# Performance work log

Measured on AMD Instinct MI355X. Metric: run time of the kernel, lower is better.

Reference implementation:

```python
import jax, jax.numpy as jnp
import numpy as np
from jax import lax

D = 512      # inter_dim
E = 768      # expand_dim
S = 256      # squeeze_dim
BUCKET = 64
N_BLOCK = 6

def layernorm(x, g, b, eps):
    m = jnp.mean(x, axis=-1, keepdims=True)
    v = jnp.mean(jnp.square(x - m), axis=-1, keepdims=True)
    return (x - m) / jnp.sqrt(v + eps) * g + b

def setup_inputs():
    key = jax.random.key(0)
    ks = jax.random.split(key, 12)
    B, N, IN = 4, 4096, 768
    def rn(k, shape, scale):
        return jax.random.normal(k, shape, dtype=jnp.float32) * scale
    return {
        "xs": jax.random.normal(ks[0], (B, N, IN), dtype=jnp.float32),
        # in1: Linear(IN, D) + LayerNorm(eps=1e-8) + LeakyReLU(0.1)
        "W_in": rn(ks[1], (IN, D), IN ** -0.5), "b_in": jnp.zeros(D),
        "ln_in_g": jnp.ones(D), "ln_in_b": jnp.zeros(D),
        # 6 GAU (FlashQuadAttention) blocks, params stacked on leading axis
        "blk_ln_g": jnp.ones((N_BLOCK, D)), "blk_ln_b": jnp.zeros((N_BLOCK, D)),
        "blk_Wuv": rn(ks[2], (N_BLOCK, D, 2 * E + S), D ** -0.5),
        "blk_buv": jnp.zeros((N_BLOCK, 2 * E + S)),
        "blk_gamma": jnp.ones((N_BLOCK, 2, S)) + rn(ks[3], (N_BLOCK, 2, S), 0.02),
        "blk_beta": rn(ks[4], (N_BLOCK, 2, S), 0.02),
        "blk_Wo": rn(ks[5], (N_BLOCK, E, D), E ** -0.5),
        "blk_bo": jnp.zeros((N_BLOCK, D)),
        # tr_layer (applied inside tree loop)
        "tr_W": rn(ks[6], (D, D), D ** -0.5), "tr_b": jnp.zeros(D),
        "tr_a": jnp.full((), 1e-6, dtype=jnp.float32),
        # out1 = TransLayer + Linear(D, out_dim)
        "tr2_W": rn(ks[7], (D, D), D ** -0.5), "tr2_b": jnp.zeros(D),
        "tr2_a": jnp.full((), 1e-6, dtype=jnp.float32),
        "out_W": rn(ks[8], (D, 2), D ** -0.5), "out_b": jnp.zeros(2),
    }

def reference(xs, W_in, b_in, ln_in_g, ln_in_b,
              blk_ln_g, blk_ln_b, blk_Wuv, blk_buv, blk_gamma, blk_beta,
              blk_Wo, blk_bo, tr_W, tr_b, tr_a, tr2_W, tr2_b, tr2_a,
              out_W, out_b):
    def subnet(h):  # h: [n_buckets, BUCKET, D]
        def step(h, p):
            lg, lb, Wuv, buv, gam, bet, Wo, bo = p
            n = layernorm(h, lg, lb, 1e-5)
            uvb = jax.nn.silu(n @ Wuv + buv)
            u, v, base = uvb[..., :E], uvb[..., E:2 * E], uvb[..., 2 * E:]
            q = base * gam[0] + bet[0]
            k = base * gam[1] + bet[1]
            Lq = h.shape[1]
            a = jnp.square(jax.nn.relu(jnp.einsum('gls,gms->glm', q, k) / Lq))
            o = jnp.einsum('glm,gme->gle', a, v) * u
            return h + o @ Wo + bo, None
        h, _ = lax.scan(step, h, (blk_ln_g, blk_ln_b, blk_Wuv, blk_buv,
                                  blk_gamma, blk_beta, blk_Wo, blk_bo))
        return h

    def tr_layer(x, W, b, a):
        return x + jax.nn.gelu(x @ W + b, approximate=False) * a

    def run_sample(x):  # x: [N, in_dim]
        h = layernorm(x @ W_in + b_in, ln_in_g, ln_in_b, 1e-8)
        h = jnp.where(h > 0, h, 0.1 * h)  # LeakyReLU(0.1)
        seq = h
        ys = []
        while seq.shape[0] > 1:  # static shapes -> unrolled tree levels
            ids = jnp.argsort(jnp.linalg.norm(seq, axis=-1))  # sort by L2 norm
            buckets = seq[ids].reshape(-1, BUCKET, D)
            gy = subnet(buckets).mean(axis=1)           # [n_buckets, D]
            ys.append(tr_layer(gy, tr_W, tr_b, tr_a).mean(axis=0))
            seq = gy
        return jnp.stack(ys, 0).mean(0)  # [D]

    y = jax.vmap(run_sample)(xs)          # [B, D]
    y = tr_layer(y, tr2_W, tr2_b, tr2_a)  # out1 TransLayer
    return y @ out_W + out_b              # [B, out_dim]
```

## Files before the change

kernel.cpp:

```cpp
#include <hip/hip_runtime.h>
#include <math.h>

#define R1C 16384

enum { OP_STORE = 0, OP_SILU = 1, OP_RESID = 2, OP_TR = 3 };

typedef _Float16 f16x8 __attribute__((ext_vector_type(8)));
typedef float f32x4 __attribute__((ext_vector_type(4)));

__device__ __forceinline__ float silu_f(float x) { return x / (1.0f + __expf(-x)); }
__device__ __forceinline__ float gelu_f(float x) {
  return 0.5f * x * (1.0f + erff(x * 0.70710678118654752f));
}

__device__ __forceinline__ void gll16(const void* g, const void* l) {
  __builtin_amdgcn_global_load_lds(
      (const __attribute__((address_space(1))) unsigned int*)g,
      (__attribute__((address_space(3))) unsigned int*)l, 16, 0, 0);
}


__global__ __launch_bounds__(512) void gemm_f16(
    const _Float16* __restrict__ A, int lda,
    const _Float16* __restrict__ Bt, int ldb,
    float* __restrict__ C, int ldc, int K,
    const float* __restrict__ bias, int mode,
    const int* __restrict__ ids)
{
  const int BUF = 128 * 32;
  __shared__ _Float16 As[2 * BUF];
  __shared__ _Float16 Bs[2 * BUF];
  int tid = threadIdx.x;
  int lane = tid & 63, w = tid >> 6;
  int wm = w >> 1, wn = w & 1;
  int row0 = blockIdx.y * 128, col0 = blockIdx.x * 128;

  int m0 = tid >> 2;
  int k0e = (((tid & 3) - (m0 >> 1)) & 3) * 8;
  const _Float16* gA0 = A + (size_t)(row0 + m0) * lda + k0e;
  const _Float16* gB0 = Bt + (size_t)(col0 + m0) * ldb + k0e;
  const _Float16* lA0 = As + (size_t)(w * 64) * 8;
  const _Float16* lB0 = Bs + (size_t)(w * 64) * 8;

  int mrow = lane & 15, quad = lane >> 4;
  const f16x8* aptr[2];
  const f16x8* bptr[4];
#pragma unroll
  for (int t = 0; t < 2; ++t) {
    int ml = wm * 32 + t * 16 + mrow;
    aptr[t] = (const f16x8*)(As + (size_t)(ml * 4 + ((quad + (ml >> 1)) & 3)) * 8);
  }
#pragma unroll
  for (int nt = 0; nt < 4; ++nt) {
    int nl = wn * 64 + nt * 16 + mrow;
    bptr[nt] = (const f16x8*)(Bs + (size_t)(nl * 4 + ((quad + (nl >> 1)) & 3)) * 8);
  }

  f32x4 acc[2][4] = {};

  gll16(gA0, lA0); gll16(gB0, lB0);
  gA0 += 32; gB0 += 32;

  for (int kt = 0; kt < K; kt += 32) {
    int cur = (kt >> 5) & 1;
    __syncthreads();
    if (kt + 32 < K) {
      int nx = cur ^ 1;
      gll16(gA0, lA0 + nx * BUF); gll16(gB0, lB0 + nx * BUF);
      gA0 += 32; gB0 += 32;
    }
    int fo = cur * (BUF / 8);
    f16x8 af[2], bfr[4];
#pragma unroll
    for (int t = 0; t < 2; ++t) af[t] = *(aptr[t] + fo);
#pragma unroll
    for (int nt = 0; nt < 4; ++nt) bfr[nt] = *(bptr[nt] + fo);
#pragma unroll
    for (int mt = 0; mt < 2; ++mt)
#pragma unroll
      for (int nt = 0; nt < 4; ++nt)
        acc[mt][nt] = __builtin_amdgcn_mfma_f32_16x16x32_f16(
            af[mt], bfr[nt], acc[mt][nt], 0, 0, 0);
  }

#pragma unroll
  for (int mt = 0; mt < 2; ++mt) {
#pragma unroll
    for (int nt = 0; nt < 4; ++nt) {
      int c = col0 + wn * 64 + nt * 16 + mrow;
      float bv = bias ? bias[c] : 0.0f;
#pragma unroll
      for (int reg = 0; reg < 4; ++reg) {
        int r = row0 + wm * 32 + mt * 16 + quad * 4 + reg;
        float val = acc[mt][nt][reg] + bv;
        if (mode == OP_STORE) {
          C[(size_t)r * ldc + c] = val;
        } else if (mode == OP_SILU) {
          C[(size_t)r * ldc + c] = silu_f(val);
        } else {
          int hr = ids ? ids[r] : r;
          C[(size_t)hr * ldc + c] += val;
        }
      }
    }
  }
}

__global__ __launch_bounds__(512) void gemm_f16_split(
    const _Float16* __restrict__ Ah, const _Float16* __restrict__ Al, int lda,
    const _Float16* __restrict__ Bh, const _Float16* __restrict__ Bl, int ldb,
    float* __restrict__ C, int ldc, int K, const float* __restrict__ bias)
{
  const int BUF = 128 * 32;
  __shared__ _Float16 AsH[2 * BUF], AsL[2 * BUF];
  __shared__ _Float16 BsH[2 * BUF], BsL[2 * BUF];
  int tid = threadIdx.x;
  int lane = tid & 63, w = tid >> 6;
  int wm = w >> 1, wn = w & 1;
  int row0 = blockIdx.y * 128, col0 = blockIdx.x * 128;

  int m0 = tid >> 2;
  int k0e = (((tid & 3) - (m0 >> 1)) & 3) * 8;
  size_t a0 = (size_t)(row0 + m0) * lda + k0e;
  size_t b0 = (size_t)(col0 + m0) * ldb + k0e;
  size_t l0 = (size_t)(w * 64) * 8;

  int mrow = lane & 15, quad = lane >> 4;
  size_t aoff[2], boff[4];
#pragma unroll
  for (int t = 0; t < 2; ++t) {
    int ml = wm * 32 + t * 16 + mrow;
    aoff[t] = (size_t)(ml * 4 + ((quad + (ml >> 1)) & 3)) * 8;
  }
#pragma unroll
  for (int nt = 0; nt < 4; ++nt) {
    int nl = wn * 64 + nt * 16 + mrow;
    boff[nt] = (size_t)(nl * 4 + ((quad + (nl >> 1)) & 3)) * 8;
  }

  f32x4 acc[2][4] = {};

  gll16(Ah + a0, AsH + l0); gll16(Al + a0, AsL + l0);
  gll16(Bh + b0, BsH + l0); gll16(Bl + b0, BsL + l0);
  a0 += 32; b0 += 32;

  for (int kt = 0; kt < K; kt += 32) {
    int cur = (kt >> 5) & 1;
    __syncthreads();
    if (kt + 32 < K) {
      size_t o = (size_t)(cur ^ 1) * BUF;
      gll16(Ah + a0, AsH + l0 + o); gll16(Al + a0, AsL + l0 + o);
      gll16(Bh + b0, BsH + l0 + o); gll16(Bl + b0, BsL + l0 + o);
      a0 += 32; b0 += 32;
    }
    size_t o = (size_t)cur * BUF;
    f16x8 ah[2], al_[2], bh[4], bl[4];
#pragma unroll
    for (int t = 0; t < 2; ++t) {
      ah[t]  = *(const f16x8*)(AsH + aoff[t] + o);
      al_[t] = *(const f16x8*)(AsL + aoff[t] + o);
    }
#pragma unroll
    for (int nt = 0; nt < 4; ++nt) {
      bh[nt] = *(const f16x8*)(BsH + boff[nt] + o);
      bl[nt] = *(const f16x8*)(BsL + boff[nt] + o);
    }
#pragma unroll
    for (int mt = 0; mt < 2; ++mt)
#pragma unroll
      for (int nt = 0; nt < 4; ++nt) {
        acc[mt][nt] = __builtin_amdgcn_mfma_f32_16x16x32_f16(
            ah[mt], bh[nt], acc[mt][nt], 0, 0, 0);
        acc[mt][nt] = __builtin_amdgcn_mfma_f32_16x16x32_f16(
            ah[mt], bl[nt], acc[mt][nt], 0, 0, 0);
        acc[mt][nt] = __builtin_amdgcn_mfma_f32_16x16x32_f16(
            al_[mt], bh[nt], acc[mt][nt], 0, 0, 0);
      }
  }

#pragma unroll
  for (int mt = 0; mt < 2; ++mt)
#pragma unroll
    for (int nt = 0; nt < 4; ++nt) {
      int c = col0 + wn * 64 + nt * 16 + mrow;
      float bv = bias ? bias[c] : 0.0f;
#pragma unroll
      for (int reg = 0; reg < 4; ++reg) {
        int r = row0 + wm * 32 + mt * 16 + quad * 4 + reg;
        C[(size_t)r * ldc + c] = acc[mt][nt][reg] + bv;
      }
    }
}

__global__ __launch_bounds__(512) void gemm_f16_uvb(
    const _Float16* __restrict__ A, int lda,
    const _Float16* __restrict__ Bt,
    int c0, int nu,
    _Float16* __restrict__ ub, _Float16* __restrict__ vb, float* __restrict__ baseb,
    int CH, int K, const float* __restrict__ buv)
{
  const int BUF = 128 * 32;
  __shared__ _Float16 As[2 * BUF];
  __shared__ _Float16 Bs[2 * BUF];
  int tid = threadIdx.x;
  int lane = tid & 63, w = tid >> 6;
  int wm = w >> 1, wn = w & 1;
  int row0 = blockIdx.y * 128;

  int x = blockIdx.x;
  int xl, regbase, ldc_, is_base = 0;
  _Float16* dst16 = nullptr;
  if (x < nu)            { xl = x;          regbase = c0;        dst16 = ub; ldc_ = CH; }
  else if (x < 2 * nu)   { xl = x - nu;     regbase = 768 + c0;  dst16 = vb; ldc_ = CH; }
  else                   { xl = x - 2 * nu; regbase = 1536;      is_base = 1; ldc_ = 256; }
  int brow0 = regbase + xl * 128;
  int dcol0 = xl * 128;

  int m0 = tid >> 2;
  int k0e = (((tid & 3) - (m0 >> 1)) & 3) * 8;
  const _Float16* gA0 = A + (size_t)(row0 + m0) * lda + k0e;
  const _Float16* gB0 = Bt + (size_t)(brow0 + m0) * 512 + k0e;
  const _Float16* lA0 = As + (size_t)(w * 64) * 8;
  const _Float16* lB0 = Bs + (size_t)(w * 64) * 8;

  int mrow = lane & 15, quad = lane >> 4;
  const f16x8* aptr[2];
  const f16x8* bptr[4];
#pragma unroll
  for (int t = 0; t < 2; ++t) {
    int ml = wm * 32 + t * 16 + mrow;
    aptr[t] = (const f16x8*)(As + (size_t)(ml * 4 + ((quad + (ml >> 1)) & 3)) * 8);
  }
#pragma unroll
  for (int nt = 0; nt < 4; ++nt) {
    int nl = wn * 64 + nt * 16 + mrow;
    bptr[nt] = (const f16x8*)(Bs + (size_t)(nl * 4 + ((quad + (nl >> 1)) & 3)) * 8);
  }

  f32x4 acc[2][4] = {};

  gll16(gA0, lA0); gll16(gB0, lB0);
  gA0 += 32; gB0 += 32;

  for (int kt = 0; kt < K; kt += 32) {
    int cur = (kt >> 5) & 1;
    __syncthreads();
    if (kt + 32 < K) {
      int nx = cur ^ 1;
      gll16(gA0, lA0 + nx * BUF); gll16(gB0, lB0 + nx * BUF);
      gA0 += 32; gB0 += 32;
    }
    int fo = cur * (BUF / 8);
    f16x8 af[2], bfr[4];
#pragma unroll
    for (int t = 0; t < 2; ++t) af[t] = *(aptr[t] + fo);
#pragma unroll
    for (int nt = 0; nt < 4; ++nt) bfr[nt] = *(bptr[nt] + fo);
#pragma unroll
    for (int mt = 0; mt < 2; ++mt)
#pragma unroll
      for (int nt = 0; nt < 4; ++nt)
        acc[mt][nt] = __builtin_amdgcn_mfma_f32_16x16x32_f16(
            af[mt], bfr[nt], acc[mt][nt], 0, 0, 0);
  }

#pragma unroll
  for (int mt = 0; mt < 2; ++mt) {
#pragma unroll
    for (int nt = 0; nt < 4; ++nt) {
      int lc = wn * 64 + nt * 16 + mrow;
      float bv = buv[brow0 + lc];
#pragma unroll
      for (int reg = 0; reg < 4; ++reg) {
        int r = row0 + wm * 32 + mt * 16 + quad * 4 + reg;
        float val = silu_f(acc[mt][nt][reg] + bv);
        if (is_base) baseb[(size_t)r * 256 + dcol0 + lc] = val;
        else         dst16[(size_t)r * ldc_ + dcol0 + lc] = (_Float16)val;
      }
    }
  }
}

__global__ __launch_bounds__(256) void attnapply_fused(
    const float* __restrict__ base, const float* __restrict__ gb,
    const float* __restrict__ bb, const _Float16* __restrict__ v,
    const _Float16* __restrict__ u, _Float16* __restrict__ t, int CH, int ech)
{
  __shared__ _Float16 smem[3 * 64 * 72];
  _Float16* qs = smem;
  _Float16* ks = smem + 64 * 72;
  _Float16* al = smem + 2 * 64 * 72;
  _Float16* vT = smem;

  int g = blockIdx.y, tid = threadIdx.x;
  int e_lo = blockIdx.x * ech, e_hi = e_lo + ech;
  int lane = tid & 63, w = tid >> 6;
  int mrow = lane & 15, quad = lane >> 4;
  int srow = tid >> 2, scol = (tid & 3) * 16;

  f32x4 acc[4] = {};
  for (int s0 = 0; s0 < 256; s0 += 64) {
    const float* bp = base + ((size_t)g * 64 + srow) * 256 + s0 + scol;
#pragma unroll
    for (int j4 = 0; j4 < 4; ++j4) {
      float4 xv = *(const float4*)(bp + j4 * 4);
      float xx[4] = {xv.x, xv.y, xv.z, xv.w};
#pragma unroll
      for (int j = 0; j < 4; ++j) {
        int s = s0 + scol + j4 * 4 + j;
        qs[srow * 72 + scol + j4 * 4 + j] = (_Float16)(xx[j] * gb[s] + bb[s]);
        ks[srow * 72 + scol + j4 * 4 + j] = (_Float16)(xx[j] * gb[256 + s] + bb[256 + s]);
      }
    }
    __syncthreads();
#pragma unroll
    for (int ks2 = 0; ks2 < 2; ++ks2) {
      f16x8 aq = *(const f16x8*)(qs + (w * 16 + mrow) * 72 + ks2 * 32 + quad * 8);
#pragma unroll
      for (int nt = 0; nt < 4; ++nt) {
        f16x8 bk = *(const f16x8*)(ks + (nt * 16 + mrow) * 72 + ks2 * 32 + quad * 8);
        acc[nt] = __builtin_amdgcn_mfma_f32_16x16x32_f16(aq, bk, acc[nt], 0, 0, 0);
      }
    }
    __syncthreads();
  }
#pragma unroll
  for (int nt = 0; nt < 4; ++nt)
#pragma unroll
    for (int reg = 0; reg < 4; ++reg) {
      float val = acc[nt][reg] * (1.0f / 64.0f);
      val = val > 0.0f ? val : 0.0f;
      val = val * val;
      al[(w * 16 + quad * 4 + reg) * 72 + nt * 16 + mrow] = (_Float16)val;
    }
  __syncthreads();

  for (int e0 = e_lo; e0 < e_hi; e0 += 64) {
    const _Float16* vp = v + ((size_t)g * 64 + srow) * CH + e0 + scol;
    f16x8 x0 = *(const f16x8*)vp;
    f16x8 x1 = *(const f16x8*)(vp + 8);
#pragma unroll
    for (int j = 0; j < 8; ++j) {
      vT[(scol + j) * 72 + srow] = x0[j];
      vT[(scol + 8 + j) * 72 + srow] = x1[j];
    }
    __syncthreads();
    f32x4 acc2[4] = {};
#pragma unroll
    for (int ks2 = 0; ks2 < 2; ++ks2) {
      f16x8 af = *(const f16x8*)(al + (w * 16 + mrow) * 72 + ks2 * 32 + quad * 8);
#pragma unroll
      for (int nt = 0; nt < 4; ++nt) {
        f16x8 bf = *(const f16x8*)(vT + (nt * 16 + mrow) * 72 + ks2 * 32 + quad * 8);
        acc2[nt] = __builtin_amdgcn_mfma_f32_16x16x32_f16(af, bf, acc2[nt], 0, 0, 0);
      }
    }
#pragma unroll
    for (int nt = 0; nt < 4; ++nt)
#pragma unroll
      for (int reg = 0; reg < 4; ++reg) {
        int row = w * 16 + quad * 4 + reg;
        int col = e0 + nt * 16 + mrow;
        size_t idx = ((size_t)g * 64 + row) * CH + col;
        t[idx] = (_Float16)(acc2[nt][reg] * (float)u[idx]);
      }
    __syncthreads();
  }
}

__global__ __launch_bounds__(256) void gemm_f32(
    const float* __restrict__ A, int lda,
    const float* __restrict__ B, int ldb,
    float* __restrict__ C, int ldc,
    int M, int N, int K,
    const float* __restrict__ bias, int mode,
    const int* __restrict__ ids,
    const float* __restrict__ X,
    const float* __restrict__ alpha)
{
  __shared__ float As[16][68];
  __shared__ float Bs[16][68];
  int tid = threadIdx.x;
  int tx = tid & 15, ty = tid >> 4;
  int col0 = blockIdx.x * 64, row0 = blockIdx.y * 64;
  float acc[4][4] = {};
  int arow = tid >> 2;
  int ak   = (tid & 3) * 4;
  int bk   = tid >> 4;
  int bn   = (tid & 15) * 4;

  for (int kt = 0; kt < K; kt += 16) {
    float4 av = make_float4(0.f, 0.f, 0.f, 0.f);
    if (row0 + arow < M)
      av = *(const float4*)&A[(size_t)(row0 + arow) * lda + kt + ak];
    As[ak + 0][arow] = av.x; As[ak + 1][arow] = av.y;
    As[ak + 2][arow] = av.z; As[ak + 3][arow] = av.w;
    float4 bv = *(const float4*)&B[(size_t)(kt + bk) * ldb + col0 + bn];
    *(float4*)&Bs[bk][bn] = bv;
    __syncthreads();
#pragma unroll
    for (int k = 0; k < 16; ++k) {
      const float4 a4 = *(const float4*)&As[k][ty * 4];
      const float4 b4 = *(const float4*)&Bs[k][tx * 4];
      float a_[4] = {a4.x, a4.y, a4.z, a4.w};
      float b_[4] = {b4.x, b4.y, b4.z, b4.w};
#pragma unroll
      for (int i = 0; i < 4; ++i)
#pragma unroll
        for (int j = 0; j < 4; ++j)
          acc[i][j] = fmaf(a_[i], b_[j], acc[i][j]);
    }
    __syncthreads();
  }

#pragma unroll
  for (int i = 0; i < 4; ++i) {
    int r = row0 + ty * 4 + i;
    if (r >= M) continue;
#pragma unroll
    for (int j = 0; j < 4; ++j) {
      int c = col0 + tx * 4 + j;
      float val = acc[i][j] + (bias ? bias[c] : 0.0f);
      if (mode == OP_STORE) {
        C[(size_t)r * ldc + c] = val;
      } else if (mode == OP_SILU) {
        C[(size_t)r * ldc + c] = silu_f(val);
      } else if (mode == OP_RESID) {
        int hr = ids ? ids[r] : r;
        C[(size_t)hr * ldc + c] += val;
      } else {
        C[(size_t)r * ldc + c] = X[(size_t)r * ldc + c] + gelu_f(val) * alpha[0];
      }
    }
  }
}

__global__ __launch_bounds__(256) void transpose_cast(
    const float* __restrict__ in, _Float16* __restrict__ out, int K, int N)
{
  in  += (size_t)blockIdx.z * K * N;
  out += (size_t)blockIdx.z * K * N;
  __shared__ float t[32][33];
  int k0 = blockIdx.y * 32, n0 = blockIdx.x * 32;
  int tx = threadIdx.x & 31, ty = threadIdx.x >> 5;
  for (int i = ty; i < 32; i += 8) {
    int k = k0 + i, n = n0 + tx;
    t[i][tx] = (k < K && n < N) ? in[(size_t)k * N + n] : 0.0f;
  }
  __syncthreads();
  for (int i = ty; i < 32; i += 8) {
    int n = n0 + i, k = k0 + tx;
    if (n < N && k < K) out[(size_t)n * K + k] = (_Float16)t[tx][i];
  }
}

__global__ __launch_bounds__(256) void transpose_split(
    const float* __restrict__ in, _Float16* __restrict__ hi,
    _Float16* __restrict__ lo, int K, int N)
{
  __shared__ float t[32][33];
  int k0 = blockIdx.y * 32, n0 = blockIdx.x * 32;
  int tx = threadIdx.x & 31, ty = threadIdx.x >> 5;
  for (int i = ty; i < 32; i += 8) {
    int k = k0 + i, n = n0 + tx;
    t[i][tx] = (k < K && n < N) ? in[(size_t)k * N + n] : 0.0f;
  }
  __syncthreads();
  for (int i = ty; i < 32; i += 8) {
    int n = n0 + i, k = k0 + tx;
    if (n < N && k < K) {
      float x = t[tx][i];
      _Float16 h = (_Float16)x;
      hi[(size_t)n * K + k] = h;
      lo[(size_t)n * K + k] = (_Float16)(x - (float)h);
    }
  }
}

__global__ __launch_bounds__(256) void split_f16_kernel(
    const float* __restrict__ in, _Float16* __restrict__ hi,
    _Float16* __restrict__ lo, int n)
{
  int i = blockIdx.x * 256 + threadIdx.x;
  if (i < n) {
    float x = in[i];
    _Float16 h = (_Float16)x;
    hi[i] = h;
    lo[i] = (_Float16)(x - (float)h);
  }
}

template <typename OUT>
__global__ __launch_bounds__(256) void ln_kernel(
    const float* __restrict__ src, const int* __restrict__ ids,
    OUT* __restrict__ dst, const float* __restrict__ g,
    const float* __restrict__ b, float eps, int leaky,
    float* __restrict__ nrm2)
{
  int r = blockIdx.x;
  int sr = ids ? ids[r] : r;
  int tid = threadIdx.x;
  float v0 = src[(size_t)sr * 512 + tid];
  float v1 = src[(size_t)sr * 512 + tid + 256];
  __shared__ float red[256], red2[256];
  red[tid] = v0 + v1;
  red2[tid] = v0 * v0 + v1 * v1;
  __syncthreads();
  for (int s = 128; s > 0; s >>= 1) {
    if (tid < s) { red[tid] += red[tid + s]; red2[tid] += red2[tid + s]; }
    __syncthreads();
  }
  float mean = red[0] * (1.0f / 512.0f);
  float var  = red2[0] * (1.0f / 512.0f) - mean * mean;
  float rs = rsqrtf(var + eps);
  float o0 = (v0 - mean) * rs * g[tid] + b[tid];
  float o1 = (v1 - mean) * rs * g[tid + 256] + b[tid + 256];
  if (leaky) {
    o0 = o0 > 0.0f ? o0 : 0.1f * o0;
    o1 = o1 > 0.0f ? o1 : 0.1f * o1;
  }
  dst[(size_t)r * 512 + tid] = (OUT)o0;
  dst[(size_t)r * 512 + tid + 256] = (OUT)o1;
  if (nrm2) {
    __syncthreads();
    red[tid] = o0 * o0 + o1 * o1;
    __syncthreads();
    for (int s = 128; s > 0; s >>= 1) {
      if (tid < s) red[tid] += red[tid + s];
      __syncthreads();
    }
    if (tid == 0) nrm2[r] = red[0];
  }
}

__global__ __launch_bounds__(128) void permute_rows(
    const float* __restrict__ src, const int* __restrict__ ids,
    float* __restrict__ dst)
{
  int r = blockIdx.x, sr = ids[r];
  const float4* s = (const float4*)(src + (size_t)sr * 512);
  float4* d = (float4*)(dst + (size_t)r * 512);
  d[threadIdx.x] = s[threadIdx.x];
}

__global__ __launch_bounds__(1024) void sort_kernel(const float* __restrict__ norm2,
                                                    int* __restrict__ ids)
{
  __shared__ float key[4096];
  __shared__ int   val[4096];
  int s = blockIdx.x, tid = threadIdx.x;
  for (int i = tid; i < 4096; i += 1024) { key[i] = norm2[s * 4096 + i]; val[i] = i; }
  __syncthreads();
  for (int len = 2; len <= 4096; len <<= 1) {
    for (int j = len >> 1; j > 0; j >>= 1) {
      for (int t = tid; t < 2048; t += 1024) {
        int i1 = (t << 1) - (t & (j - 1));
        int i2 = i1 + j;
        bool up = ((i1 & len) == 0);
        float ka = key[i1], kb = key[i2];
        int va = val[i1], vb = val[i2];
        bool gt = (ka > kb) || (ka == kb && va > vb);
        if (gt == up) {
          key[i1] = kb; key[i2] = ka;
          val[i1] = vb; val[i2] = va;
        }
      }
      __syncthreads();
    }
  }
  for (int i = tid; i < 4096; i += 1024) ids[s * 4096 + i] = s * 4096 + val[i];
}

__global__ __launch_bounds__(256) void bucketmean_kernel(
    const float* __restrict__ src, const int* __restrict__ ids,
    float* __restrict__ dst)
{
  int g = blockIdx.x, tid = threadIdx.x;
  float s0 = 0.0f, s1 = 0.0f;
  for (int i = 0; i < 64; ++i) {
    int r = g * 64 + i;
    if (ids) r = ids[r];
    s0 += src[(size_t)r * 512 + tid];
    s1 += src[(size_t)r * 512 + tid + 256];
  }
  dst[(size_t)g * 512 + tid] = s0 * (1.0f / 64.0f);
  dst[(size_t)g * 512 + tid + 256] = s1 * (1.0f / 64.0f);
}

__global__ void avg_kernel(const float* __restrict__ a, const float* __restrict__ b,
                           float* __restrict__ o, int n)
{
  int i = blockIdx.x * 256 + threadIdx.x;
  if (i < n) o[i] = 0.5f * (a[i] + b[i]);
}

__global__ void out_kernel(const float* __restrict__ y, const float* __restrict__ W,
                           const float* __restrict__ b, float* __restrict__ out)
{
  int tid = threadIdx.x;
  if (tid < 8) {
    int s = tid >> 1, j = tid & 1;
    float acc = b[j];
    for (int d = 0; d < 512; ++d) acc += y[s * 512 + d] * W[d * 2 + j];
    out[s * 2 + j] = acc;
  }
}

extern "C" void kernel_launch(void* const* d_in, const int* in_sizes, int n_in,
                              void* d_out, int out_size, void* d_ws, size_t ws_size,
                              hipStream_t stream)
{
  const float* xs       = (const float*)d_in[0];
  const float* W_in     = (const float*)d_in[1];
  const float* b_in     = (const float*)d_in[2];
  const float* ln_in_g  = (const float*)d_in[3];
  const float* ln_in_b  = (const float*)d_in[4];
  const float* blk_ln_g = (const float*)d_in[5];
  const float* blk_ln_b = (const float*)d_in[6];
  const float* blk_Wuv  = (const float*)d_in[7];
  const float* blk_buv  = (const float*)d_in[8];
  const float* blk_gam  = (const float*)d_in[9];
  const float* blk_bet  = (const float*)d_in[10];
  const float* blk_Wo   = (const float*)d_in[11];
  const float* blk_bo   = (const float*)d_in[12];
  const float* tr_W     = (const float*)d_in[13];
  const float* tr_b     = (const float*)d_in[14];
  const float* tr_a     = (const float*)d_in[15];
  const float* tr2_W    = (const float*)d_in[16];
  const float* tr2_b    = (const float*)d_in[17];
  const float* tr2_a    = (const float*)d_in[18];
  const float* out_W    = (const float*)d_in[19];
  const float* out_b    = (const float*)d_in[20];
  float* outp = (float*)d_out;

  const size_t R1 = R1C;

  char* wsb = (char*)d_ws;
  size_t off = 0;
  auto carve = [&](size_t bytes) {
    char* r = wsb + off;
    off = (off + bytes + 255) & ~(size_t)255;
    return (void*)r;
  };
  float* h      = (float*)carve(R1 * 512 * 4);
  float* hslot  = (float*)carve(R1 * 512 * 4);
  float* norm2b = (float*)carve(R1 * 4);
  int*   idsb   = (int*)carve(R1 * 4);
  float* gy     = (float*)carve((size_t)256 * 512 * 4);
  float* tl     = (float*)carve((size_t)256 * 512 * 4);
  float* gy2    = (float*)carve(4 * 512 * 4);
  float* ys0    = (float*)carve(4 * 512 * 4);
  float* ys1    = (float*)carve(4 * 512 * 4);
  float* yv     = (float*)carve(4 * 512 * 4);
  float* y2     = (float*)carve(4 * 512 * 4);
  _Float16* Wuvt = (_Float16*)carve((size_t)6 * 1792 * 512 * 2);
  _Float16* Wot  = (_Float16*)carve((size_t)6 * 512 * 768 * 2);
  size_t persistent = off;

  size_t stageA_sorted = 2 * R1 * 768 * 2 + 2 * (size_t)512 * 768 * 2 + R1 * 512 * 4 + 2048;
  size_t block768 = R1 * 256 * 4 + 3 * R1 * (size_t)768 * 2 + 2048;
  size_t un_sorted = stageA_sorted > block768 ? stageA_sorted : block768;
  bool sorted_mode = (persistent + un_sorted + 4096 <= ws_size);

  int CH = 768;
  bool splitA = true;
  if (!sorted_mode) {
    size_t stageA_fb = 2 * R1 * 768 * 2 + 2 * (size_t)512 * 768 * 2 + 1024;
    auto block_bytes = [&](size_t ch) {
      return R1 * 256 * 4 + 3 * R1 * ch * 2 + 2048;
    };
    CH = 0; splitA = false;
    const int cand[4] = {768, 384, 256, 128};
    for (int ci = 0; ci < 4; ++ci) {
      size_t bb2 = block_bytes(cand[ci]);
      size_t un2 = bb2 > stageA_fb ? bb2 : stageA_fb;
      if (persistent + un2 + 4096 <= ws_size) { CH = cand[ci]; splitA = true; break; }
    }
    if (!CH) {
      for (int ci = 0; ci < 4; ++ci)
        if (persistent + block_bytes(cand[ci]) + 4096 <= ws_size) { CH = cand[ci]; break; }
      if (!CH) CH = 128;
    }
  }
  int nu = CH / 128;
  int ech = CH >= 256 ? 256 : CH;
  int nch = CH / ech;

  char* un = wsb + ((persistent + 255) & ~(size_t)255);
  _Float16* xs_hi = (_Float16*)un;
  _Float16* xs_lo = xs_hi + R1 * 768;
  _Float16* Wt_hi = xs_lo + R1 * 768;
  _Float16* Wt_lo = Wt_hi + (size_t)512 * 768;
  float*    nbA   = sorted_mode ? (float*)(Wt_lo + (size_t)512 * 768) : hslot;
  float*    baseb = (float*)un;
  _Float16* ub    = (_Float16*)(un + R1 * 256 * 4);
  _Float16* vb    = ub + R1 * (size_t)CH;
  _Float16* tb    = vb + R1 * (size_t)CH;
  _Float16* nbuf  = sorted_mode ? tb : (_Float16*)hslot;
  float* hres = sorted_mode ? hslot : h;
  const int* blkids = sorted_mode ? nullptr : idsb;

  dim3 blk(256);
  dim3 blk5(512);

  transpose_cast<<<dim3(56, 16, 6), blk, 0, stream>>>(blk_Wuv, Wuvt, 512, 1792);
  transpose_cast<<<dim3(16, 24, 6), blk, 0, stream>>>(blk_Wo, Wot, 768, 512);

  if (splitA) {
    split_f16_kernel<<<(int)(R1 * 768 / 256), blk, 0, stream>>>(xs, xs_hi, xs_lo,
                                                                (int)(R1 * 768));
    transpose_split<<<dim3(16, 24, 1), blk, 0, stream>>>(W_in, Wt_hi, Wt_lo, 768, 512);
    gemm_f16_split<<<dim3(4, 128), blk5, 0, stream>>>(xs_hi, xs_lo, 768,
        Wt_hi, Wt_lo, 768, nbA, 512, 768, b_in);
  } else {
    gemm_f32<<<dim3(8, 256), blk, 0, stream>>>(xs, 768, W_in, 512, nbA, 512,
        16384, 512, 768, b_in, OP_STORE, nullptr, nullptr, nullptr);
  }
  ln_kernel<float><<<16384, 256, 0, stream>>>(nbA, nullptr, h, ln_in_g, ln_in_b,
                                              1e-8f, 1, norm2b);
  sort_kernel<<<4, 1024, 0, stream>>>(norm2b, idsb);
  if (sorted_mode)
    permute_rows<<<16384, 128, 0, stream>>>(h, idsb, hres);

  for (int b = 0; b < 6; ++b) {
    const _Float16* Wuv_t = Wuvt + (size_t)b * 1792 * 512;
    const float*    buv   = blk_buv + b * 1792;
    const _Float16* Wo_t  = Wot + (size_t)b * 512 * 768;
    ln_kernel<_Float16><<<16384, 256, 0, stream>>>(hres, blkids, nbuf,
        blk_ln_g + b * 512, blk_ln_b + b * 512, 1e-5f, 0, nullptr);
    for (int c0 = 0; c0 < 768; c0 += CH) {
      int incl = (c0 == 0) ? 2 : 0;
      gemm_f16_uvb<<<dim3(2 * nu + incl, 128), blk5, 0, stream>>>(nbuf, 512, Wuv_t,
          c0, nu, ub, vb, baseb, CH, 512, buv);
      attnapply_fused<<<dim3(nch, 256), blk, 0, stream>>>(baseb, blk_gam + b * 512,
          blk_bet + b * 512, vb, ub, tb, CH, ech);
      const float* bo = (c0 + CH == 768) ? (blk_bo + b * 512) : nullptr;
      gemm_f16<<<dim3(4, 128), blk5, 0, stream>>>(tb, CH, Wo_t + c0, 768,
          hres, 512, CH, bo, OP_RESID, blkids);
    }
  }
  bucketmean_kernel<<<256, 256, 0, stream>>>(hres, blkids, gy);

  gemm_f32<<<dim3(8, 4), blk, 0, stream>>>(gy, 512, tr_W, 512, tl, 512,
      256, 512, 512, tr_b, OP_TR, nullptr, gy, tr_a);
  bucketmean_kernel<<<4, 256, 0, stream>>>(tl, nullptr, ys0);

  for (int b = 0; b < 6; ++b) {
    const _Float16* Wuv_t = Wuvt + (size_t)b * 1792 * 512;
    const float*    buv   = blk_buv + b * 1792;
    const _Float16* Wo_t  = Wot + (size_t)b * 512 * 768;
    ln_kernel<_Float16><<<256, 256, 0, stream>>>(gy, nullptr, nbuf, blk_ln_g + b * 512,
                                                 blk_ln_b + b * 512, 1e-5f, 0, nullptr);
    for (int c0 = 0; c0 < 768; c0 += CH) {
      int incl = (c0 == 0) ? 2 : 0;
      gemm_f16_uvb<<<dim3(2 * nu + incl, 2), blk5, 0, stream>>>(nbuf, 512, Wuv_t,
          c0, nu, ub, vb, baseb, CH, 512, buv);
      attnapply_fused<<<dim3(nch, 4), blk, 0, stream>>>(baseb, blk_gam + b * 512,
          blk_bet + b * 512, vb, ub, tb, CH, ech);
      const float* bo = (c0 + CH == 768) ? (blk_bo + b * 512) : nullptr;
      gemm_f16<<<dim3(4, 2), blk5, 0, stream>>>(tb, CH, Wo_t + c0, 768,
          gy, 512, CH, bo, OP_RESID, nullptr);
    }
  }
  bucketmean_kernel<<<4, 256, 0, stream>>>(gy, nullptr, gy2);

  gemm_f32<<<dim3(8, 1), blk, 0, stream>>>(gy2, 512, tr_W, 512, ys1, 512,
      4, 512, 512, tr_b, OP_TR, nullptr, gy2, tr_a);
  avg_kernel<<<8, 256, 0, stream>>>(ys0, ys1, yv, 2048);
  gemm_f32<<<dim3(8, 1), blk, 0, stream>>>(yv, 512, tr2_W, 512, y2, 512,
      4, 512, 512, tr2_b, OP_TR, nullptr, yv, tr2_a);
  out_kernel<<<1, 64, 0, stream>>>(y2, out_W, out_b, outp);
}
```

Baseline: 1.614 ms.

## Use 4-wave 128x128 GEMM tiles with 4x4 MFMA per wave and XCD swizzle

The f16 GEMM kernels move from 8 waves (512 threads) to 4 waves (256 threads) on the same 128x128 tile. Each wave now computes a 64x64 sub-tile with 4x4 MFMA accumulators, and each thread issues two async global-to-LDS loads per operand. This raises register reuse per LDS fragment load and lowers per-block thread overhead, at the cost of more accumulator registers per thread. An XCD-aware block index remap is also added to the GEMMs and the attention kernel so neighbouring tiles share L2 on the same chiplet.

```diff
diff --git a/kernel.cpp b/kernel.cpp
--- a/kernel.cpp
+++ b/kernel.cpp
@@ -19,8 +19,20 @@
       (__attribute__((address_space(3))) unsigned int*)l, 16, 0, 0);
 }
 
-
-__global__ __launch_bounds__(512) void gemm_f16(
+__device__ __forceinline__ void xcd_swizzle(int& bx, int& by) {
+  int nx = gridDim.x;
+  int nwg = nx * gridDim.y;
+  int flat = by * nx + bx;
+  int q = nwg >> 3, r = nwg & 7;
+  int xcd = flat & 7, pos = flat >> 3;
+  int lbid = (xcd < r) ? xcd * (q + 1) + pos
+                       : r * (q + 1) + (xcd - r) * q + pos;
+  bx = lbid % nx;
+  by = lbid / nx;
+}
+
+
+__global__ __launch_bounds__(256) void gemm_f16(
     const _Float16* __restrict__ A, int lda,
     const _Float16* __restrict__ Bt, int ldb,
     float* __restrict__ C, int ldc, int K,
@@ -30,53 +42,56 @@
   const int BUF = 128 * 32;
   __shared__ _Float16 As[2 * BUF];
   __shared__ _Float16 Bs[2 * BUF];
+  int bx = blockIdx.x, by = blockIdx.y;
+  xcd_swizzle(bx, by);
   int tid = threadIdx.x;
   int lane = tid & 63, w = tid >> 6;
   int wm = w >> 1, wn = w & 1;
-  int row0 = blockIdx.y * 128, col0 = blockIdx.x * 128;
-
-  int m0 = tid >> 2;
-  int k0e = (((tid & 3) - (m0 >> 1)) & 3) * 8;
-  const _Float16* gA0 = A + (size_t)(row0 + m0) * lda + k0e;
-  const _Float16* gB0 = Bt + (size_t)(col0 + m0) * ldb + k0e;
-  const _Float16* lA0 = As + (size_t)(w * 64) * 8;
-  const _Float16* lB0 = Bs + (size_t)(w * 64) * 8;
+  int row0 = by * 128, col0 = bx * 128;
+
+  int sm0 = tid >> 2;
+  int sk  = (((tid & 3) - (sm0 >> 1)) & 3) * 8;
+  const _Float16* gA[2];
+  const _Float16* gB[2];
+  gA[0] = A + (size_t)(row0 + sm0) * lda + sk;
+  gA[1] = A + (size_t)(row0 + 64 + sm0) * lda + sk;
+  gB[0] = Bt + (size_t)(col0 + sm0) * ldb + sk;
+  gB[1] = Bt + (size_t)(col0 + 64 + sm0) * ldb + sk;
+  const _Float16* lA[2] = { As + (size_t)(w * 64) * 8, As + (size_t)(256 + w * 64) * 8 };
+  const _Float16* lB[2] = { Bs + (size_t)(w * 64) * 8, Bs + (size_t)(256 + w * 64) * 8 };
 
   int mrow = lane & 15, quad = lane >> 4;
-  const f16x8* aptr[2];
+  const f16x8* aptr[4];
   const f16x8* bptr[4];
 #pragma unroll
-  for (int t = 0; t < 2; ++t) {
-    int ml = wm * 32 + t * 16 + mrow;
+  for (int t = 0; t < 4; ++t) {
+    int ml = wm * 64 + t * 16 + mrow;
     aptr[t] = (const f16x8*)(As + (size_t)(ml * 4 + ((quad + (ml >> 1)) & 3)) * 8);
-  }
-#pragma unroll
-  for (int nt = 0; nt < 4; ++nt) {
-    int nl = wn * 64 + nt * 16 + mrow;
-    bptr[nt] = (const f16x8*)(Bs + (size_t)(nl * 4 + ((quad + (nl >> 1)) & 3)) * 8);
-  }
-
-  f32x4 acc[2][4] = {};
-
-  gll16(gA0, lA0); gll16(gB0, lB0);
-  gA0 += 32; gB0 += 32;
+    int nl = wn * 64 + t * 16 + mrow;
+    bptr[t] = (const f16x8*)(Bs + (size_t)(nl * 4 + ((quad + (nl >> 1)) & 3)) * 8);
+  }
+
+  f32x4 acc[4][4] = {};
+
+  gll16(gA[0], lA[0]); gll16(gA[1], lA[1]);
+  gll16(gB[0], lB[0]); gll16(gB[1], lB[1]);
+  gA[0] += 32; gA[1] += 32; gB[0] += 32; gB[1] += 32;
 
   for (int kt = 0; kt < K; kt += 32) {
     int cur = (kt >> 5) & 1;
     __syncthreads();
     if (kt + 32 < K) {
-      int nx = cur ^ 1;
-      gll16(gA0, lA0 + nx * BUF); gll16(gB0, lB0 + nx * BUF);
-      gA0 += 32; gB0 += 32;
+      int nxo = (cur ^ 1) * BUF;
+      gll16(gA[0], lA[0] + nxo); gll16(gA[1], lA[1] + nxo);
+      gll16(gB[0], lB[0] + nxo); gll16(gB[1], lB[1] + nxo);
+      gA[0] += 32; gA[1] += 32; gB[0] += 32; gB[1] += 32;
     }
     int fo = cur * (BUF / 8);
-    f16x8 af[2], bfr[4];
-#pragma unroll
-    for (int t = 0; t < 2; ++t) af[t] = *(aptr[t] + fo);
-#pragma unroll
-    for (int nt = 0; nt < 4; ++nt) bfr[nt] = *(bptr[nt] + fo);
-#pragma unroll
-    for (int mt = 0; mt < 2; ++mt)
+    f16x8 af[4], bfr[4];
+#pragma unroll
+    for (int t = 0; t < 4; ++t) { af[t] = *(aptr[t] + fo); bfr[t] = *(bptr[t] + fo); }
+#pragma unroll
+    for (int mt = 0; mt < 4; ++mt)
 #pragma unroll
       for (int nt = 0; nt < 4; ++nt)
         acc[mt][nt] = __builtin_amdgcn_mfma_f32_16x16x32_f16(
@@ -84,14 +99,14 @@
   }
 
 #pragma unroll
-  for (int mt = 0; mt < 2; ++mt) {
+  for (int mt = 0; mt < 4; ++mt) {
 #pragma unroll
     for (int nt = 0; nt < 4; ++nt) {
       int c = col0 + wn * 64 + nt * 16 + mrow;
       float bv = bias ? bias[c] : 0.0f;
 #pragma unroll
       for (int reg = 0; reg < 4; ++reg) {
-        int r = row0 + wm * 32 + mt * 16 + quad * 4 + reg;
+        int r = row0 + wm * 64 + mt * 16 + quad * 4 + reg;
         float val = acc[mt][nt][reg] + bv;
         if (mode == OP_STORE) {
           C[(size_t)r * ldc + c] = val;
@@ -114,10 +129,12 @@
   const int BUF = 128 * 32;
   __shared__ _Float16 AsH[2 * BUF], AsL[2 * BUF];
   __shared__ _Float16 BsH[2 * BUF], BsL[2 * BUF];
+  int bx = blockIdx.x, by = blockIdx.y;
+  xcd_swizzle(bx, by);
   int tid = threadIdx.x;
   int lane = tid & 63, w = tid >> 6;
   int wm = w >> 1, wn = w & 1;
-  int row0 = blockIdx.y * 128, col0 = blockIdx.x * 128;
+  int row0 = by * 128, col0 = bx * 128;
 
   int m0 = tid >> 2;
   int k0e = (((tid & 3) - (m0 >> 1)) & 3) * 8;
@@ -192,7 +209,7 @@
     }
 }
 
-__global__ __launch_bounds__(512) void gemm_f16_uvb(
+__global__ __launch_bounds__(256) void gemm_f16_uvb(
     const _Float16* __restrict__ A, int lda,
     const _Float16* __restrict__ Bt,
     int c0, int nu,
@@ -202,12 +219,14 @@
   const int BUF = 128 * 32;
   __shared__ _Float16 As[2 * BUF];
   __shared__ _Float16 Bs[2 * BUF];
+  int bx = blockIdx.x, by = blockIdx.y;
+  xcd_swizzle(bx, by);
   int tid = threadIdx.x;
   int lane = tid & 63, w = tid >> 6;
   int wm = w >> 1, wn = w & 1;
-  int row0 = blockIdx.y * 128;
-
-  int x = blockIdx.x;
+  int row0 = by * 128;
+
+  int x = bx;
   int xl, regbase, ldc_, is_base = 0;
   _Float16* dst16 = nullptr;
   if (x < nu)            { xl = x;          regbase = c0;        dst16 = ub; ldc_ = CH; }
@@ -216,48 +235,49 @@
   int brow0 = regbase + xl * 128;
   int dcol0 = xl * 128;
 
-  int m0 = tid >> 2;
-  int k0e = (((tid & 3) - (m0 >> 1)) & 3) * 8;
-  const _Float16* gA0 = A + (size_t)(row0 + m0) * lda + k0e;
-  const _Float16* gB0 = Bt + (size_t)(brow0 + m0) * 512 + k0e;
-  const _Float16* lA0 = As + (size_t)(w * 64) * 8;
-  const _Float16* lB0 = Bs + (size_t)(w * 64) * 8;
+  int sm0 = tid >> 2;
+  int sk  = (((tid & 3) - (sm0 >> 1)) & 3) * 8;
+  const _Float16* gA[2];
+  const _Float16* gB[2];
+  gA[0] = A + (size_t)(row0 + sm0) * lda + sk;
+  gA[1] = A + (size_t)(row0 + 64 + sm0) * lda + sk;
+  gB[0] = Bt + (size_t)(brow0 + sm0) * 512 + sk;
+  gB[1] = Bt + (size_t)(brow0 + 64 + sm0) * 512 + sk;
+  const _Float16* lA[2] = { As + (size_t)(w * 64) * 8, As + (size_t)(256 + w * 64) * 8 };
+  const _Float16* lB[2] = { Bs + (size_t)(w * 64) * 8, Bs + (size_t)(256 + w * 64) * 8 };
 
   int mrow = lane & 15, quad = lane >> 4;
-  const f16x8* aptr[2];
+  const f16x8* aptr[4];
   const f16x8* bptr[4];
 #pragma unroll
-  for (int t = 0; t < 2; ++t) {
-    int ml = wm * 32 + t * 16 + mrow;
+  for (int t = 0; t < 4; ++t) {
+    int ml = wm * 64 + t * 16 + mrow;
     aptr[t] = (const f16x8*)(As + (size_t)(ml * 4 + ((quad + (ml >> 1)) & 3)) * 8);
-  }
-#pragma unroll
-  for (int nt = 0; nt < 4; ++nt) {
-    int nl = wn * 64 + nt * 16 + mrow;
-    bptr[nt] = (const f16x8*)(Bs + (size_t)(nl * 4 + ((quad + (nl >> 1)) & 3)) * 8);
-  }
-
-  f32x4 acc[2][4] = {};
-
-  gll16(gA0, lA0); gll16(gB0, lB0);
-  gA0 += 32; gB0 += 32;
+    int nl = wn * 64 + t * 16 + mrow;
+    bptr[t] = (const f16x8*)(Bs + (size_t)(nl * 4 + ((quad + (nl >> 1)) & 3)) * 8);
+  }
+
+  f32x4 acc[4][4] = {};
+
+  gll16(gA[0], lA[0]); gll16(gA[1], lA[1]);
+  gll16(gB[0], lB[0]); gll16(gB[1], lB[1]);
+  gA[0] += 32; gA[1] += 32; gB[0] += 32; gB[1] += 32;
 
   for (int kt = 0; kt < K; kt += 32) {
     int cur = (kt >> 5) & 1;
     __syncthreads();
     if (kt + 32 < K) {
-      int nx = cur ^ 1;
-      gll16(gA0, lA0 + nx * BUF); gll16(gB0, lB0 + nx * BUF);
-      gA0 += 32; gB0 += 32;
+      int nxo = (cur ^ 1) * BUF;
+      gll16(gA[0], lA[0] + nxo); gll16(gA[1], lA[1] + nxo);
+      gll16(gB[0], lB[0] + nxo); gll16(gB[1], lB[1] + nxo);
+      gA[0] += 32; gA[1] += 32; gB[0] += 32; gB[1] += 32;
     }
     int fo = cur * (BUF / 8);
-    f16x8 af[2], bfr[4];
-#pragma unroll
-    for (int t = 0; t < 2; ++t) af[t] = *(aptr[t] + fo);
-#pragma unroll
-    for (int nt = 0; nt < 4; ++nt) bfr[nt] = *(bptr[nt] + fo);
-#pragma unroll
-    for (int mt = 0; mt < 2; ++mt)
+    f16x8 af[4], bfr[4];
+#pragma unroll
+    for (int t = 0; t < 4; ++t) { af[t] = *(aptr[t] + fo); bfr[t] = *(bptr[t] + fo); }
+#pragma unroll
+    for (int mt = 0; mt < 4; ++mt)
 #pragma unroll
       for (int nt = 0; nt < 4; ++nt)
         acc[mt][nt] = __builtin_amdgcn_mfma_f32_16x16x32_f16(
@@ -265,14 +285,14 @@
   }
 
 #pragma unroll
-  for (int mt = 0; mt < 2; ++mt) {
+  for (int mt = 0; mt < 4; ++mt) {
 #pragma unroll
     for (int nt = 0; nt < 4; ++nt) {
       int lc = wn * 64 + nt * 16 + mrow;
       float bv = buv[brow0 + lc];
 #pragma unroll
       for (int reg = 0; reg < 4; ++reg) {
-        int r = row0 + wm * 32 + mt * 16 + quad * 4 + reg;
+        int r = row0 + wm * 64 + mt * 16 + quad * 4 + reg;
         float val = silu_f(acc[mt][nt][reg] + bv);
         if (is_base) baseb[(size_t)r * 256 + dcol0 + lc] = val;
         else         dst16[(size_t)r * ldc_ + dcol0 + lc] = (_Float16)val;
@@ -292,8 +312,10 @@
   _Float16* al = smem + 2 * 64 * 72;
   _Float16* vT = smem;
 
-  int g = blockIdx.y, tid = threadIdx.x;
-  int e_lo = blockIdx.x * ech, e_hi = e_lo + ech;
+  int bx = blockIdx.x, by = blockIdx.y;
+  xcd_swizzle(bx, by);
+  int g = by, tid = threadIdx.x;
+  int e_lo = bx * ech, e_hi = e_lo + ech;
   int lane = tid & 63, w = tid >> 6;
   int mrow = lane & 15, quad = lane >> 4;
   int srow = tid >> 2, scol = (tid & 3) * 16;
@@ -730,12 +752,12 @@
         blk_ln_g + b * 512, blk_ln_b + b * 512, 1e-5f, 0, nullptr);
     for (int c0 = 0; c0 < 768; c0 += CH) {
       int incl = (c0 == 0) ? 2 : 0;
-      gemm_f16_uvb<<<dim3(2 * nu + incl, 128), blk5, 0, stream>>>(nbuf, 512, Wuv_t,
+      gemm_f16_uvb<<<dim3(2 * nu + incl, 128), blk, 0, stream>>>(nbuf, 512, Wuv_t,
           c0, nu, ub, vb, baseb, CH, 512, buv);
       attnapply_fused<<<dim3(nch, 256), blk, 0, stream>>>(baseb, blk_gam + b * 512,
           blk_bet + b * 512, vb, ub, tb, CH, ech);
       const float* bo = (c0 + CH == 768) ? (blk_bo + b * 512) : nullptr;
-      gemm_f16<<<dim3(4, 128), blk5, 0, stream>>>(tb, CH, Wo_t + c0, 768,
+      gemm_f16<<<dim3(4, 128), blk, 0, stream>>>(tb, CH, Wo_t + c0, 768,
           hres, 512, CH, bo, OP_RESID, blkids);
     }
   }
@@ -753,12 +775,12 @@
                                                  blk_ln_b + b * 512, 1e-5f, 0, nullptr);
     for (int c0 = 0; c0 < 768; c0 += CH) {
       int incl = (c0 == 0) ? 2 : 0;
-      gemm_f16_uvb<<<dim3(2 * nu + incl, 2), blk5, 0, stream>>>(nbuf, 512, Wuv_t,
+      gemm_f16_uvb<<<dim3(2 * nu + incl, 2), blk, 0, stream>>>(nbuf, 512, Wuv_t,
           c0, nu, ub, vb, baseb, CH, 512, buv);
       attnapply_fused<<<dim3(nch, 4), blk, 0, stream>>>(baseb, blk_gam + b * 512,
           blk_bet + b * 512, vb, ub, tb, CH, ech);
       const float* bo = (c0 + CH == 768) ? (blk_bo + b * 512) : nullptr;
-      gemm_f16<<<dim3(4, 2), blk5, 0, stream>>>(tb, CH, Wo_t + c0, 768,
+      gemm_f16<<<dim3(4, 2), blk, 0, stream>>>(tb, CH, Wo_t + c0, 768,
           gy, 512, CH, bo, OP_RESID, nullptr);
     }
   }
```

New measurement: 1.747 ms. 1.08x slower.

## Triple-buffer GEMM LDS pipeline with vmcnt waits and XCD-aware block swizzle

Applied to the files above, without the earlier changes.

The two main f16 GEMM kernels move from a double-buffered LDS scheme with __syncthreads to a three-stage ring, prefetching two K-tiles ahead. Each iteration waits only on the tile it needs via explicit s_waitcnt vmcnt plus a raw barrier, so more global loads are in flight while MFMAs run. Separately, block indices in all GEMMs and the attention kernel are remapped so consecutive logical tiles land on the same XCD, aiming for better L2 reuse. The risks are higher LDS use per block, which may lower occupancy, and the vmcnt counts silently depending on exactly two gll16 loads per stage.

```diff
diff --git a/kernel.cpp b/kernel.cpp
--- a/kernel.cpp
+++ b/kernel.cpp
@@ -17,6 +17,18 @@
   __builtin_amdgcn_global_load_lds(
       (const __attribute__((address_space(1))) unsigned int*)g,
       (__attribute__((address_space(3))) unsigned int*)l, 16, 0, 0);
+}
+
+__device__ __forceinline__ void xcd_swizzle(int& bx, int& by) {
+  int nx = gridDim.x;
+  int nwg = nx * gridDim.y;
+  int flat = by * nx + bx;
+  int q = nwg >> 3, r = nwg & 7;
+  int xcd = flat & 7, pos = flat >> 3;
+  int lbid = (xcd < r) ? xcd * (q + 1) + pos
+                       : r * (q + 1) + (xcd - r) * q + pos;
+  bx = lbid % nx;
+  by = lbid / nx;
 }
 
 
@@ -28,12 +40,14 @@
     const int* __restrict__ ids)
 {
   const int BUF = 128 * 32;
-  __shared__ _Float16 As[2 * BUF];
-  __shared__ _Float16 Bs[2 * BUF];
+  __shared__ _Float16 As[3 * BUF];
+  __shared__ _Float16 Bs[3 * BUF];
+  int bx = blockIdx.x, by = blockIdx.y;
+  xcd_swizzle(bx, by);
   int tid = threadIdx.x;
   int lane = tid & 63, w = tid >> 6;
   int wm = w >> 1, wn = w & 1;
-  int row0 = blockIdx.y * 128, col0 = blockIdx.x * 128;
+  int row0 = by * 128, col0 = bx * 128;
 
   int m0 = tid >> 2;
   int k0e = (((tid & 3) - (m0 >> 1)) & 3) * 8;
@@ -58,21 +72,29 @@
 
   f32x4 acc[2][4] = {};
 
+  int ntile = K >> 5;
   gll16(gA0, lA0); gll16(gB0, lB0);
   gA0 += 32; gB0 += 32;
-
-  for (int kt = 0; kt < K; kt += 32) {
-    int cur = (kt >> 5) & 1;
-    __syncthreads();
-    if (kt + 32 < K) {
-      int nx = cur ^ 1;
-      gll16(gA0, lA0 + nx * BUF); gll16(gB0, lB0 + nx * BUF);
+  if (ntile > 1) {
+    gll16(gA0, lA0 + BUF); gll16(gB0, lB0 + BUF);
+    gA0 += 32; gB0 += 32;
+  }
+
+  int cur = 0;
+  for (int t = 0; t < ntile; ++t) {
+    if (t + 1 < ntile) asm volatile("s_waitcnt vmcnt(2)" ::: "memory");
+    else               asm volatile("s_waitcnt vmcnt(0)" ::: "memory");
+    __builtin_amdgcn_s_barrier();
+    __builtin_amdgcn_sched_barrier(0);
+    if (t + 2 < ntile) {
+      int pf = cur + 2; if (pf >= 3) pf -= 3;
+      gll16(gA0, lA0 + pf * BUF); gll16(gB0, lB0 + pf * BUF);
       gA0 += 32; gB0 += 32;
     }
     int fo = cur * (BUF / 8);
     f16x8 af[2], bfr[4];
 #pragma unroll
-    for (int t = 0; t < 2; ++t) af[t] = *(aptr[t] + fo);
+    for (int tt = 0; tt < 2; ++tt) af[tt] = *(aptr[tt] + fo);
 #pragma unroll
     for (int nt = 0; nt < 4; ++nt) bfr[nt] = *(bptr[nt] + fo);
 #pragma unroll
@@ -81,6 +103,7 @@
       for (int nt = 0; nt < 4; ++nt)
         acc[mt][nt] = __builtin_amdgcn_mfma_f32_16x16x32_f16(
             af[mt], bfr[nt], acc[mt][nt], 0, 0, 0);
+    cur = (cur == 2) ? 0 : cur + 1;
   }
 
 #pragma unroll
@@ -114,10 +137,12 @@
   const int BUF = 128 * 32;
   __shared__ _Float16 AsH[2 * BUF], AsL[2 * BUF];
   __shared__ _Float16 BsH[2 * BUF], BsL[2 * BUF];
+  int bx = blockIdx.x, by = blockIdx.y;
+  xcd_swizzle(bx, by);
   int tid = threadIdx.x;
   int lane = tid & 63, w = tid >> 6;
   int wm = w >> 1, wn = w & 1;
-  int row0 = blockIdx.y * 128, col0 = blockIdx.x * 128;
+  int row0 = by * 128, col0 = bx * 128;
 
   int m0 = tid >> 2;
   int k0e = (((tid & 3) - (m0 >> 1)) & 3) * 8;
@@ -200,14 +225,16 @@
     int CH, int K, const float* __restrict__ buv)
 {
   const int BUF = 128 * 32;
-  __shared__ _Float16 As[2 * BUF];
-  __shared__ _Float16 Bs[2 * BUF];
+  __shared__ _Float16 As[3 * BUF];
+  __shared__ _Float16 Bs[3 * BUF];
+  int bx = blockIdx.x, by = blockIdx.y;
+  xcd_swizzle(bx, by);
   int tid = threadIdx.x;
   int lane = tid & 63, w = tid >> 6;
   int wm = w >> 1, wn = w & 1;
-  int row0 = blockIdx.y * 128;
-
-  int x = blockIdx.x;
+  int row0 = by * 128;
+
+  int x = bx;
   int xl, regbase, ldc_, is_base = 0;
   _Float16* dst16 = nullptr;
   if (x < nu)            { xl = x;          regbase = c0;        dst16 = ub; ldc_ = CH; }
@@ -239,21 +266,29 @@
 
   f32x4 acc[2][4] = {};
 
+  int ntile = K >> 5;
   gll16(gA0, lA0); gll16(gB0, lB0);
   gA0 += 32; gB0 += 32;
-
-  for (int kt = 0; kt < K; kt += 32) {
-    int cur = (kt >> 5) & 1;
-    __syncthreads();
-    if (kt + 32 < K) {
-      int nx = cur ^ 1;
-      gll16(gA0, lA0 + nx * BUF); gll16(gB0, lB0 + nx * BUF);
+  if (ntile > 1) {
+    gll16(gA0, lA0 + BUF); gll16(gB0, lB0 + BUF);
+    gA0 += 32; gB0 += 32;
+  }
+
+  int cur = 0;
+  for (int t = 0; t < ntile; ++t) {
+    if (t + 1 < ntile) asm volatile("s_waitcnt vmcnt(2)" ::: "memory");
+    else               asm volatile("s_waitcnt vmcnt(0)" ::: "memory");
+    __builtin_amdgcn_s_barrier();
+    __builtin_amdgcn_sched_barrier(0);
+    if (t + 2 < ntile) {
+      int pf = cur + 2; if (pf >= 3) pf -= 3;
+      gll16(gA0, lA0 + pf * BUF); gll16(gB0, lB0 + pf * BUF);
       gA0 += 32; gB0 += 32;
     }
     int fo = cur * (BUF / 8);
     f16x8 af[2], bfr[4];
 #pragma unroll
-    for (int t = 0; t < 2; ++t) af[t] = *(aptr[t] + fo);
+    for (int tt = 0; tt < 2; ++tt) af[tt] = *(aptr[tt] + fo);
 #pragma unroll
     for (int nt = 0; nt < 4; ++nt) bfr[nt] = *(bptr[nt] + fo);
 #pragma unroll
@@ -262,6 +297,7 @@
       for (int nt = 0; nt < 4; ++nt)
         acc[mt][nt] = __builtin_amdgcn_mfma_f32_16x16x32_f16(
             af[mt], bfr[nt], acc[mt][nt], 0, 0, 0);
+    cur = (cur == 2) ? 0 : cur + 1;
   }
 
 #pragma unroll
@@ -292,8 +328,10 @@
   _Float16* al = smem + 2 * 64 * 72;
   _Float16* vT = smem;
 
-  int g = blockIdx.y, tid = threadIdx.x;
-  int e_lo = blockIdx.x * ech, e_hi = e_lo + ech;
+  int bx = blockIdx.x, by = blockIdx.y;
+  xcd_swizzle(bx, by);
+  int g = by, tid = threadIdx.x;
+  int e_lo = bx * ech, e_hi = e_lo + ech;
   int lane = tid & 63, w = tid >> 6;
   int mrow = lane & 15, quad = lane >> 4;
   int srow = tid >> 2, scol = (tid & 3) * 16;
```

New measurement: 1.595 ms. Within noise of the previous version (-1.2%).
